# Kernel tuning notes

Measured on AMD Instinct MI355X. Metric: run time of the kernel, lower is better.

The kernel has to match this reference:

```python
import jax, jax.numpy as jnp
import numpy as np

# dims per init_kwargs / input_specs
B, C, H, W = 8, 256, 56, 56
K = 3            # kernel_size
S = 1            # stride
D = 1            # dilation
HEAD = 1
MID = int(C * 0.2)   # se_ratio bottleneck = 51
GAIN = float(np.sqrt(2.0))  # calculate_gain('relu')


def setup_inputs() -> dict:
    key = jax.random.key(0)
    ks = jax.random.split(key, 6)
    sc = 0.05
    return {
        "x": jax.random.normal(ks[0], (B, C, H, W), jnp.float32),
        # channel branch: 1x1 convs stored as dense matrices
        "w1": jax.random.normal(ks[1], (MID, C), jnp.float32) * sc,
        "b1": jnp.zeros((MID,), jnp.float32),
        "w2": jax.random.normal(ks[2], (C * K * K, MID), jnp.float32) * sc,
        "b2": jnp.zeros((C * K * K,), jnp.float32),
        # spatial branch: 1x1 conv c -> head*k^2
        "ws": jax.random.normal(ks[3], (HEAD * K * K, C), jnp.float32) * sc,
        "bs": jnp.zeros((HEAD * K * K,), jnp.float32),
        # FilterNorm running_std parameter (channel branch): randn * gain/k
        "fn_std": jax.random.normal(ks[4], (C * K * K,), jnp.float32) * (GAIN / K),
    }


def _ddf_mul(x, cf, sf):
    """Decoupled dynamic filter, 'mul' combine.
    x: (B,C,H,W), cf: (B,C,K,K) channel filter, sf: (B,K*K,Ho,Wo) spatial filter.
    out[b,c,i,j] = sum_{u,v} x[b,c, i*S+(u-(K-1)/2)*D, j*S+(v-(K-1)/2)*D] * cf[b,c,u,v] * sf[b,u*K+v,i,j]
    Accumulate over the K*K taps to avoid materializing the unfolded tensor."""
    p = D * (K - 1) // 2
    xp = jnp.pad(x, ((0, 0), (0, 0), (p, p), (p, p)))
    Ho, Wo = H // S, W // S
    out = jnp.zeros((B, C, Ho, Wo), x.dtype)
    for u in range(K):
        for v in range(K):
            patch = xp[:, :, u * D:u * D + S * Ho:S, v * D:v * D + S * Wo:S]
            out = out + patch * cf[:, :, u, v][:, :, None, None] * sf[:, u * K + v][:, None]
    return out


def reference(x, w1, b1, w2, b2, ws, bs, fn_std):
    # ---- channel branch: SE-style filter generation ----
    pooled = x.mean((2, 3))                                  # (B,C) global avg pool
    y = jax.nn.relu(pooled @ w1.T + b1)                      # (B,MID)
    y = (y @ w2.T + b2).reshape(B, C, K * K)                 # (B,C,K^2)
    # FilterNorm 'channel': normalize over K^2 (torch std -> ddof=1), learned std
    y = (y - y.mean(-1, keepdims=True)) / (y.std(-1, ddof=1, keepdims=True) + 1e-10)
    cf = (y.reshape(B, C * K * K) * fn_std).reshape(B, C, K, K)
    # ---- spatial branch: 1x1 conv (stride S) + FilterNorm 'spatial' ----
    xs = x[:, :, ::S, ::S]
    sf = jnp.einsum('bchw,nc->bnhw', xs, ws) + bs[None, :, None, None]  # (B,K^2,Ho,Wo)
    sf = sf.reshape(B, HEAD, K * K, H // S, W // S)
    sf = (sf - sf.mean(2, keepdims=True)) / (sf.std(2, ddof=1, keepdims=True) + 1e-10)
    sf = sf.reshape(B, HEAD * K * K, H // S, W // S) * (GAIN / K)
    # ---- fused per-pixel gather-multiply-reduce (head=1 -> no group reshape) ----
    return _ddf_mul(x, cf, sf)
```

## Files before the change

### kernel.cpp

```cpp
#include <hip/hip_runtime.h>
#include <math.h>

#define BB   8
#define CC   256
#define HH   56
#define WW   56
#define KK   3
#define MIDN 51
#define NTAP (KK*KK)
#define CKK  (CC*NTAP)
#define HW   (HH*WW)
#define SPIX 64
#define NSTR (HW/SPIX)
#define CPR  128
#define XSTR 65
#define NCPB 4
#define TILE 3364

__global__ __launch_bounds__(256) void k_sf(const float* __restrict__ x,
                                            const float* __restrict__ ws,
                                            const float* __restrict__ bs,
                                            float* __restrict__ sf,
                                            float* __restrict__ poolpart) {
    int blk = blockIdx.x;
    int s = blk % NSTR;
    int b = blk / NSTR;
    int t = threadIdx.x;
    int p = t & 63;
    int q = t >> 6;
    __shared__ float xs[CPR * XSTR];
    __shared__ float wss[NTAP][CC];
    __shared__ float accq[NTAP * 4 * SPIX];
    for (int idx = t; idx < NTAP * CC; idx += 256)
        ((float*)wss)[idx] = ws[idx];
    float acc[NTAP];
    #pragma unroll
    for (int n = 0; n < NTAP; ++n) acc[n] = 0.f;
    const float* xb = x + ((size_t)b * CC) * HW + s * SPIX;
    #pragma unroll
    for (int r = 0; r < 2; ++r) {
        if (r) __syncthreads();
        float vv[32];
        #pragma unroll
        for (int c = 0; c < 32; ++c)
            vv[c] = xb[(size_t)(r * CPR + q * 32 + c) * HW + p];
        #pragma unroll
        for (int c = 0; c < 32; ++c)
            xs[(q * 32 + c) * XSTR + p] = vv[c];
        __syncthreads();
        if (t < CPR) {
            float sum = 0.f;
            #pragma unroll 8
            for (int pp = 0; pp < SPIX; ++pp) sum += xs[t * XSTR + pp];
            poolpart[((size_t)(b * NSTR + s)) * CC + r * CPR + t] = sum;
        }
        #pragma unroll 4
        for (int c = 0; c < 32; ++c) {
            float xv = xs[(q * 32 + c) * XSTR + p];
            #pragma unroll
            for (int n = 0; n < NTAP; ++n)
                acc[n] += xv * wss[n][r * CPR + q * 32 + c];
        }
    }
    #pragma unroll
    for (int n = 0; n < NTAP; ++n) accq[(n * 4 + q) * SPIX + p] = acc[n];
    __syncthreads();
    if (t < SPIX) {
        float y[NTAP];
        #pragma unroll
        for (int n = 0; n < NTAP; ++n) {
            float v = bs[n];
            #pragma unroll
            for (int qq = 0; qq < 4; ++qq) v += accq[(n * 4 + qq) * SPIX + t];
            y[n] = v;
        }
        float mean = 0.f;
        #pragma unroll
        for (int n = 0; n < NTAP; ++n) mean += y[n];
        mean *= (1.f / NTAP);
        float var = 0.f;
        #pragma unroll
        for (int n = 0; n < NTAP; ++n) { float d = y[n] - mean; var += d * d; }
        float inv = 0.47140452079103173f /
                    (sqrtf(var * (1.f / (NTAP - 1))) + 1e-10f);
        #pragma unroll
        for (int n = 0; n < NTAP; ++n)
            sf[((size_t)(b * NTAP + n)) * HW + s * SPIX + t] = (y[n] - mean) * inv;
    }
}

#define MLPBLK (BB*8)
#define CPC 32
#define W2CHUNK (CPC*NTAP*MIDN)
__global__ __launch_bounds__(256) void k_mlp(const float* __restrict__ poolpart,
                                             const float* __restrict__ w1,
                                             const float* __restrict__ b1,
                                             const float* __restrict__ w2,
                                             const float* __restrict__ b2,
                                             const float* __restrict__ fn_std,
                                             float* __restrict__ cf) {
    __shared__ float smem[W2CHUNK + 256 + 64 + CPC * NTAP];
    float* w2s = smem;
    float* ps  = smem + W2CHUNK;
    float* y1  = ps + 256;
    float* y2s = y1 + 64;
    int blk = blockIdx.x;
    int t = threadIdx.x;
    int b = blk >> 3, chunk = blk & 7;
    int c0 = chunk * CPC;
    const float4* w2v = (const float4*)(w2 + (size_t)chunk * W2CHUNK);
    float4* w2s4 = (float4*)w2s;
    for (int i = t; i < W2CHUNK / 4; i += 256) w2s4[i] = w2v[i];
    {
        float s = 0.f;
        const float* pp = poolpart + ((size_t)b * NSTR) * CC + t;
        for (int st = 0; st < NSTR; ++st) s += pp[(size_t)st * CC];
        ps[t] = s * (1.0f / HW);
    }
    __syncthreads();
    if (t < MIDN) {
        float acc = b1[t];
        const float* wr = w1 + t * CC;
        for (int c2 = 0; c2 < CC; ++c2) acc += ps[c2] * wr[c2];
        y1[t] = fmaxf(acc, 0.f);
    }
    __syncthreads();
    #pragma unroll
    for (int base = 0; base < 512; base += 256) {
        int idx = base + t;
        if (idx < CPC * NTAP) {
            float acc = b2[c0 * NTAP + idx];
            const float* r = w2s + idx * MIDN;
            #pragma unroll 3
            for (int m = 0; m < MIDN; ++m) acc += y1[m] * r[m];
            y2s[idx] = acc;
        }
    }
    __syncthreads();
    if (t < CPC) {
        int c = c0 + t;
        float y2[NTAP];
        #pragma unroll
        for (int qq = 0; qq < NTAP; ++qq) y2[qq] = y2s[t * NTAP + qq];
        float mean = 0.f;
        #pragma unroll
        for (int qq = 0; qq < NTAP; ++qq) mean += y2[qq];
        mean *= (1.f / NTAP);
        float var = 0.f;
        #pragma unroll
        for (int qq = 0; qq < NTAP; ++qq) { float d = y2[qq] - mean; var += d * d; }
        float inv = 1.f / (sqrtf(var * (1.f / (NTAP - 1))) + 1e-10f);
        #pragma unroll
        for (int qq = 0; qq < NTAP; ++qq) {
            int idx = c * NTAP + qq;
            cf[(size_t)b * CKK + idx] = (y2[qq] - mean) * inv * fn_std[idx];
        }
    }
}

__global__ __launch_bounds__(512) void k_ddf(const float* __restrict__ x,
                                             const float* __restrict__ cf,
                                             const float* __restrict__ sf,
                                             float* __restrict__ out) {
    int blk = blockIdx.x;
    int b = blk / (CC / NCPB), cg = blk % (CC / NCPB);
    int c0 = cg * NCPB;
    int t = threadIdx.x;
    __shared__ float xt[NCPB][TILE];
    for (int idx = t; idx < NCPB * TILE; idx += 512) ((float*)xt)[idx] = 0.f;
    __syncthreads();
    const float4* xp4 = (const float4*)(x + ((size_t)(b * CC + c0)) * HW);
    for (int i4 = t; i4 < NCPB * HW / 4; i4 += 512) {
        float4 v = xp4[i4];
        int k = i4 / (HW / 4);
        int rem4 = i4 - k * (HW / 4);
        int r = rem4 / (WW / 4);
        int col = 4 * (rem4 - r * (WW / 4));
        float* d = &xt[k][(r + 1) * 58 + col + 1];
        d[0] = v.x; d[1] = v.y; d[2] = v.z; d[3] = v.w;
    }
    float cf9[NCPB][NTAP];
    const float* cfp = cf + (size_t)b * CKK + c0 * NTAP;
    #pragma unroll
    for (int k = 0; k < NCPB; ++k)
        #pragma unroll
        for (int n = 0; n < NTAP; ++n) cf9[k][n] = cfp[k * NTAP + n];
    __syncthreads();
    const float* sfb = sf + (size_t)b * NTAP * HW;
    float* op = out + ((size_t)(b * CC + c0)) * HW;
    for (int idx = t; idx < HW; idx += 512) {
        int i = idx / WW, j = idx - i * WW;
        float s9[NTAP];
        #pragma unroll
        for (int n = 0; n < NTAP; ++n) s9[n] = sfb[(size_t)n * HW + idx];
        float acc[NCPB];
        #pragma unroll
        for (int k = 0; k < NCPB; ++k) acc[k] = 0.f;
        #pragma unroll
        for (int u = 0; u < KK; ++u)
            #pragma unroll
            for (int v = 0; v < KK; ++v) {
                int n = u * KK + v;
                int o = (i + u) * 58 + (j + v);
                #pragma unroll
                for (int k = 0; k < NCPB; ++k)
                    acc[k] += xt[k][o] * (cf9[k][n] * s9[n]);
            }
        #pragma unroll
        for (int k = 0; k < NCPB; ++k) op[(size_t)k * HW + idx] = acc[k];
    }
}

extern "C" void kernel_launch(void* const* d_in, const int* in_sizes, int n_in,
                              void* d_out, int out_size, void* d_ws, size_t ws_size,
                              hipStream_t stream) {
    const float* x      = (const float*)d_in[0];
    const float* w1     = (const float*)d_in[1];
    const float* b1     = (const float*)d_in[2];
    const float* w2     = (const float*)d_in[3];
    const float* b2     = (const float*)d_in[4];
    const float* ws     = (const float*)d_in[5];
    const float* bs     = (const float*)d_in[6];
    const float* fn_std = (const float*)d_in[7];
    float* out = (float*)d_out;

    float* wsf      = (float*)d_ws;
    float* cf       = wsf;
    float* sf       = cf + 18432;
    float* poolpart = sf + 225792;

    k_sf<<<BB * NSTR, 256, 0, stream>>>(x, ws, bs, sf, poolpart);
    k_mlp<<<MLPBLK, 256, 0, stream>>>(poolpart, w1, b1, w2, b2, fn_std, cf);
    k_ddf<<<BB * (CC / NCPB), 512, 0, stream>>>(x, cf, sf, out);
}
```

Before: 118.4 us.

## Register-tile ddf stencil: 7 pixels per thread with row-reuse and aligned float4 smem

Restructures the ddf stencil kernel so each of 448 threads computes a 7-pixel strip of one row for all 4 channels. Each tap row of x is held in registers and reused across neighbouring output pixels. Spatial filter values are loaded once per strip. The padded shared tile gets a 68-float row stride so staging can use aligned float4 stores and zeroing can be vectorised. The cost is more registers per thread, which could lower occupancy, and strided 7-element global accesses for sf and out that may coalesce poorly.

```diff
diff --git a/kernel.cpp b/kernel.cpp
--- a/kernel.cpp
+++ b/kernel.cpp
@@ -15,7 +15,8 @@
 #define CPR  128
 #define XSTR 65
 #define NCPB 4
-#define TILE 3364
+#define TROW 68
+#define TPL  (58*TROW)
 
 __global__ __launch_bounds__(256) void k_sf(const float* __restrict__ x,
                                             const float* __restrict__ ws,
@@ -158,7 +159,7 @@
     }
 }
 
-__global__ __launch_bounds__(512) void k_ddf(const float* __restrict__ x,
+__global__ __launch_bounds__(448) void k_ddf(const float* __restrict__ x,
                                              const float* __restrict__ cf,
                                              const float* __restrict__ sf,
                                              float* __restrict__ out) {
@@ -166,18 +167,21 @@
     int b = blk / (CC / NCPB), cg = blk % (CC / NCPB);
     int c0 = cg * NCPB;
     int t = threadIdx.x;
-    __shared__ float xt[NCPB][TILE];
-    for (int idx = t; idx < NCPB * TILE; idx += 512) ((float*)xt)[idx] = 0.f;
+    __shared__ __align__(16) float xt[NCPB][TPL];
+    {
+        float4 z4 = make_float4(0.f, 0.f, 0.f, 0.f);
+        float4* xt4 = (float4*)xt;
+        for (int i4 = t; i4 < NCPB * TPL / 4; i4 += 448) xt4[i4] = z4;
+    }
     __syncthreads();
     const float4* xp4 = (const float4*)(x + ((size_t)(b * CC + c0)) * HW);
-    for (int i4 = t; i4 < NCPB * HW / 4; i4 += 512) {
+    for (int i4 = t; i4 < NCPB * HW / 4; i4 += 448) {
         float4 v = xp4[i4];
         int k = i4 / (HW / 4);
         int rem4 = i4 - k * (HW / 4);
         int r = rem4 / (WW / 4);
         int col = 4 * (rem4 - r * (WW / 4));
-        float* d = &xt[k][(r + 1) * 58 + col + 1];
-        d[0] = v.x; d[1] = v.y; d[2] = v.z; d[3] = v.w;
+        *(float4*)&xt[k][(r + 1) * TROW + col + 4] = v;
     }
     float cf9[NCPB][NTAP];
     const float* cfp = cf + (size_t)b * CKK + c0 * NTAP;
@@ -186,29 +190,43 @@
         #pragma unroll
         for (int n = 0; n < NTAP; ++n) cf9[k][n] = cfp[k * NTAP + n];
     __syncthreads();
-    const float* sfb = sf + (size_t)b * NTAP * HW;
-    float* op = out + ((size_t)(b * CC + c0)) * HW;
-    for (int idx = t; idx < HW; idx += 512) {
-        int i = idx / WW, j = idx - i * WW;
-        float s9[NTAP];
-        #pragma unroll
-        for (int n = 0; n < NTAP; ++n) s9[n] = sfb[(size_t)n * HW + idx];
-        float acc[NCPB];
-        #pragma unroll
-        for (int k = 0; k < NCPB; ++k) acc[k] = 0.f;
-        #pragma unroll
-        for (int u = 0; u < KK; ++u)
-            #pragma unroll
-            for (int v = 0; v < KK; ++v) {
-                int n = u * KK + v;
-                int o = (i + u) * 58 + (j + v);
-                #pragma unroll
-                for (int k = 0; k < NCPB; ++k)
-                    acc[k] += xt[k][o] * (cf9[k][n] * s9[n]);
-            }
-        #pragma unroll
-        for (int k = 0; k < NCPB; ++k) op[(size_t)k * HW + idx] = acc[k];
-    }
+    int row = t >> 3;
+    int j0 = (t & 7) * 7;
+    const float* sfb = sf + (size_t)b * NTAP * HW + row * WW + j0;
+    float acc[NCPB][7];
+    #pragma unroll
+    for (int k = 0; k < NCPB; ++k)
+        #pragma unroll
+        for (int jj = 0; jj < 7; ++jj) acc[k][jj] = 0.f;
+    #pragma unroll
+    for (int u = 0; u < KK; ++u) {
+        float sfv[3][7];
+        #pragma unroll
+        for (int v = 0; v < 3; ++v)
+            #pragma unroll
+            for (int jj = 0; jj < 7; ++jj)
+                sfv[v][jj] = sfb[(size_t)(u * 3 + v) * HW + jj];
+        int base = (row + u) * TROW + j0 + 3;
+        #pragma unroll
+        for (int k = 0; k < NCPB; ++k) {
+            float xr[9];
+            #pragma unroll
+            for (int m = 0; m < 9; ++m) xr[m] = xt[k][base + m];
+            float c_0 = cf9[k][u * 3 + 0];
+            float c_1 = cf9[k][u * 3 + 1];
+            float c_2 = cf9[k][u * 3 + 2];
+            #pragma unroll
+            for (int jj = 0; jj < 7; ++jj)
+                acc[k][jj] += xr[jj]     * (c_0 * sfv[0][jj])
+                            + xr[jj + 1] * (c_1 * sfv[1][jj])
+                            + xr[jj + 2] * (c_2 * sfv[2][jj]);
+        }
+    }
+    float* op = out + ((size_t)(b * CC + c0)) * HW + row * WW + j0;
+    #pragma unroll
+    for (int k = 0; k < NCPB; ++k)
+        #pragma unroll
+        for (int jj = 0; jj < 7; ++jj) op[(size_t)k * HW + jj] = acc[k][jj];
 }
 
 extern "C" void kernel_launch(void* const* d_in, const int* in_sizes, int n_in,
@@ -231,5 +249,5 @@
 
     k_sf<<<BB * NSTR, 256, 0, stream>>>(x, ws, bs, sf, poolpart);
     k_mlp<<<MLPBLK, 256, 0, stream>>>(poolpart, w1, b1, w2, b2, fn_std, cf);
-    k_ddf<<<BB * (CC / NCPB), 512, 0, stream>>>(x, cf, sf, out);
-}
+    k_ddf<<<BB * (CC / NCPB), 448, 0, stream>>>(x, cf, sf, out);
+}
```

New measurement: 121.4 us. +2.6%, slower.

## Fuse SE MLP channel-filter generation into the DDF kernel

Applied to the files above, without the earlier changes.

Removes the separate k_mlp launch and has each k_ddf block recompute the pooled mean, the first MLP layer, and just the 36 rows of the second layer it needs, writing the normalized channel filter to shared memory. This drops one kernel launch and the global cf round trip. In exchange, the pooling reduction and the full 51x256 first layer are recomputed redundantly in all 512 blocks, and three extra barriers plus serial per-thread loops sit before the main stencil loop.

```diff
diff --git a/kernel.cpp b/kernel.cpp
--- a/kernel.cpp
+++ b/kernel.cpp
@@ -89,77 +89,13 @@
     }
 }
 
-#define MLPBLK (BB*8)
-#define CPC 32
-#define W2CHUNK (CPC*NTAP*MIDN)
-__global__ __launch_bounds__(256) void k_mlp(const float* __restrict__ poolpart,
+__global__ __launch_bounds__(512) void k_ddf(const float* __restrict__ x,
+                                             const float* __restrict__ poolpart,
                                              const float* __restrict__ w1,
                                              const float* __restrict__ b1,
                                              const float* __restrict__ w2,
                                              const float* __restrict__ b2,
                                              const float* __restrict__ fn_std,
-                                             float* __restrict__ cf) {
-    __shared__ float smem[W2CHUNK + 256 + 64 + CPC * NTAP];
-    float* w2s = smem;
-    float* ps  = smem + W2CHUNK;
-    float* y1  = ps + 256;
-    float* y2s = y1 + 64;
-    int blk = blockIdx.x;
-    int t = threadIdx.x;
-    int b = blk >> 3, chunk = blk & 7;
-    int c0 = chunk * CPC;
-    const float4* w2v = (const float4*)(w2 + (size_t)chunk * W2CHUNK);
-    float4* w2s4 = (float4*)w2s;
-    for (int i = t; i < W2CHUNK / 4; i += 256) w2s4[i] = w2v[i];
-    {
-        float s = 0.f;
-        const float* pp = poolpart + ((size_t)b * NSTR) * CC + t;
-        for (int st = 0; st < NSTR; ++st) s += pp[(size_t)st * CC];
-        ps[t] = s * (1.0f / HW);
-    }
-    __syncthreads();
-    if (t < MIDN) {
-        float acc = b1[t];
-        const float* wr = w1 + t * CC;
-        for (int c2 = 0; c2 < CC; ++c2) acc += ps[c2] * wr[c2];
-        y1[t] = fmaxf(acc, 0.f);
-    }
-    __syncthreads();
-    #pragma unroll
-    for (int base = 0; base < 512; base += 256) {
-        int idx = base + t;
-        if (idx < CPC * NTAP) {
-            float acc = b2[c0 * NTAP + idx];
-            const float* r = w2s + idx * MIDN;
-            #pragma unroll 3
-            for (int m = 0; m < MIDN; ++m) acc += y1[m] * r[m];
-            y2s[idx] = acc;
-        }
-    }
-    __syncthreads();
-    if (t < CPC) {
-        int c = c0 + t;
-        float y2[NTAP];
-        #pragma unroll
-        for (int qq = 0; qq < NTAP; ++qq) y2[qq] = y2s[t * NTAP + qq];
-        float mean = 0.f;
-        #pragma unroll
-        for (int qq = 0; qq < NTAP; ++qq) mean += y2[qq];
-        mean *= (1.f / NTAP);
-        float var = 0.f;
-        #pragma unroll
-        for (int qq = 0; qq < NTAP; ++qq) { float d = y2[qq] - mean; var += d * d; }
-        float inv = 1.f / (sqrtf(var * (1.f / (NTAP - 1))) + 1e-10f);
-        #pragma unroll
-        for (int qq = 0; qq < NTAP; ++qq) {
-            int idx = c * NTAP + qq;
-            cf[(size_t)b * CKK + idx] = (y2[qq] - mean) * inv * fn_std[idx];
-        }
-    }
-}
-
-__global__ __launch_bounds__(512) void k_ddf(const float* __restrict__ x,
-                                             const float* __restrict__ cf,
                                              const float* __restrict__ sf,
                                              float* __restrict__ out) {
     int blk = blockIdx.x;
@@ -167,6 +103,10 @@
     int c0 = cg * NCPB;
     int t = threadIdx.x;
     __shared__ float xt[NCPB][TILE];
+    __shared__ float ps[CC];
+    __shared__ float y1s[64];
+    __shared__ float y2s[NCPB * NTAP];
+    __shared__ float cfs[NCPB * NTAP];
     for (int idx = t; idx < NCPB * TILE; idx += 512) ((float*)xt)[idx] = 0.f;
     __syncthreads();
     const float4* xp4 = (const float4*)(x + ((size_t)(b * CC + c0)) * HW);
@@ -179,13 +119,51 @@
         float* d = &xt[k][(r + 1) * 58 + col + 1];
         d[0] = v.x; d[1] = v.y; d[2] = v.z; d[3] = v.w;
     }
+    if (t < CC) {
+        float s = 0.f;
+        const float* pp = poolpart + ((size_t)b * NSTR) * CC + t;
+        for (int st = 0; st < NSTR; ++st) s += pp[(size_t)st * CC];
+        ps[t] = s * (1.0f / HW);
+    }
+    __syncthreads();
+    if (t < MIDN) {
+        float a = b1[t];
+        const float* wr = w1 + t * CC;
+        for (int c2 = 0; c2 < CC; ++c2) a += ps[c2] * wr[c2];
+        y1s[t] = fmaxf(a, 0.f);
+    }
+    __syncthreads();
+    if (t < NCPB * NTAP) {
+        int row = c0 * NTAP + t;
+        float a = b2[row];
+        const float* r = w2 + (size_t)row * MIDN;
+        #pragma unroll 3
+        for (int m = 0; m < MIDN; ++m) a += y1s[m] * r[m];
+        y2s[t] = a;
+    }
+    __syncthreads();
+    if (t < NCPB) {
+        float y2[NTAP];
+        #pragma unroll
+        for (int q = 0; q < NTAP; ++q) y2[q] = y2s[t * NTAP + q];
+        float mean = 0.f;
+        #pragma unroll
+        for (int q = 0; q < NTAP; ++q) mean += y2[q];
+        mean *= (1.f / NTAP);
+        float var = 0.f;
+        #pragma unroll
+        for (int q = 0; q < NTAP; ++q) { float d = y2[q] - mean; var += d * d; }
+        float inv = 1.f / (sqrtf(var * (1.f / (NTAP - 1))) + 1e-10f);
+        #pragma unroll
+        for (int q = 0; q < NTAP; ++q)
+            cfs[t * NTAP + q] = (y2[q] - mean) * inv * fn_std[(c0 + t) * NTAP + q];
+    }
+    __syncthreads();
     float cf9[NCPB][NTAP];
-    const float* cfp = cf + (size_t)b * CKK + c0 * NTAP;
     #pragma unroll
     for (int k = 0; k < NCPB; ++k)
         #pragma unroll
-        for (int n = 0; n < NTAP; ++n) cf9[k][n] = cfp[k * NTAP + n];
-    __syncthreads();
+        for (int n = 0; n < NTAP; ++n) cf9[k][n] = cfs[k * NTAP + n];
     const float* sfb = sf + (size_t)b * NTAP * HW;
     float* op = out + ((size_t)(b * CC + c0)) * HW;
     for (int idx = t; idx < HW; idx += 512) {
@@ -225,11 +203,10 @@
     float* out = (float*)d_out;
 
     float* wsf      = (float*)d_ws;
-    float* cf       = wsf;
-    float* sf       = cf + 18432;
+    float* sf       = wsf;
     float* poolpart = sf + 225792;
 
     k_sf<<<BB * NSTR, 256, 0, stream>>>(x, ws, bs, sf, poolpart);
-    k_mlp<<<MLPBLK, 256, 0, stream>>>(poolpart, w1, b1, w2, b2, fn_std, cf);
-    k_ddf<<<BB * (CC / NCPB), 512, 0, stream>>>(x, cf, sf, out);
+    k_ddf<<<BB * (CC / NCPB), 512, 0, stream>>>(x, poolpart, w1, b1, w2, b2,
+                                                fn_std, sf, out);
 }
```

New measurement: 114.9 us (median of 2 runs). -2.9%, faster.
